# Kernel optimization log

Measured on AMD Instinct MI355X. Metric: run time of the kernel, lower is better.

Reference implementation:

```python
import jax, jax.numpy as jnp
import numpy as np

# ---- config (mirrors DecodeSSDPredictions init kwargs) ----
IMG_H, IMG_W = 512, 512
NMS_MAX = 100          # nms_max_output_size: greedy NMS iterations
CONF_T = 0.5           # confidence_threshold
IOU_T = 0.35           # iou_threshold
NUM_PRED = 10          # num_predictions (final top-k)
B, N_BOXES, N_CLASSES = 32, 24564, 81  # class 0 = background


def setup_inputs() -> dict:
    key = jax.random.key(0)
    k1, k2, k3, k4 = jax.random.split(key, 4)
    # class confidences: softmax of sharp logits so a fraction pass conf>=0.5
    cls = jax.nn.softmax(jax.random.normal(k1, (B, N_BOXES, N_CLASSES), jnp.float32) * 3.0, axis=-1)
    # predicted offsets (cx, cy, log w, log h deltas)
    offsets = jax.random.normal(k2, (B, N_BOXES, 4), jnp.float32) * 0.5
    # anchor priors: centers in (0,1), sizes in (0.05, 0.3)
    cxcy = jax.random.uniform(k3, (B, N_BOXES, 2), jnp.float32, 0.05, 0.95)
    wh = jax.random.uniform(k4, (B, N_BOXES, 2), jnp.float32, 0.05, 0.30)
    variances = jnp.broadcast_to(jnp.array([0.1, 0.1, 0.2, 0.2], jnp.float32), (B, N_BOXES, 4))
    y_pred = jnp.concatenate([cls, offsets, cxcy, wh, variances], axis=-1)  # [B, N, C+12]
    return {"y_pred": y_pred}


def _iou(boxes, box):
    # boxes: [N,4] corners (xmin,ymin,xmax,ymax); box: [4]
    iw = jnp.clip(jnp.minimum(boxes[:, 2], box[2]) - jnp.maximum(boxes[:, 0], box[0]), 0.0)
    ih = jnp.clip(jnp.minimum(boxes[:, 3], box[3]) - jnp.maximum(boxes[:, 1], box[1]), 0.0)
    inter = iw * ih
    area_b = (boxes[:, 2] - boxes[:, 0]) * (boxes[:, 3] - boxes[:, 1])
    area_q = (box[2] - box[0]) * (box[3] - box[1])
    return inter / (area_b + area_q - inter + 1e-12)


def _per_item(rows6):
    # rows6: [N, 6] = (class_id, score, xmin, ymin, xmax, ymax)
    neg_inf = jnp.float32(-jnp.inf)
    valid = (rows6[:, 0] != 0) & (rows6[:, 1] >= CONF_T)  # drop background + low conf
    scores0 = jnp.where(valid, rows6[:, 1], neg_inf)
    boxes = rows6[:, 2:6]

    def body(i, carry):
        alive, kept_idx, kept_sc = carry
        idx = jnp.argmax(alive)
        best = alive[idx]
        ok = best > neg_inf
        kept_idx = kept_idx.at[i].set(jnp.where(ok, idx.astype(jnp.int32), -1))
        kept_sc = kept_sc.at[i].set(jnp.where(ok, best, neg_inf))
        # suppress overlapping boxes (incl. the selected one, iou=1 > thr)
        sup = _iou(boxes, boxes[idx]) > IOU_T
        alive = jnp.where(ok & sup, neg_inf, alive)
        return alive, kept_idx, kept_sc

    carry0 = (scores0,
              jnp.full((NMS_MAX,), -1, jnp.int32),
              jnp.full((NMS_MAX,), neg_inf, jnp.float32))
    _, kept_idx, kept_sc = jax.lax.fori_loop(0, NMS_MAX, body, carry0)

    kept_rows = rows6[jnp.clip(kept_idx, 0)]            # [NMS_MAX, 6]
    top_sc, top_i = jax.lax.top_k(kept_sc, NUM_PRED)    # final top-k by score
    out = kept_rows[top_i]
    return jnp.where(jnp.isfinite(top_sc)[:, None], out, 0.0)


def reference(y_pred):
    cls = y_pred[..., :-12]
    # SSD box decode
    cx = y_pred[..., -12] * y_pred[..., -4] * y_pred[..., -6] + y_pred[..., -8]
    cy = y_pred[..., -11] * y_pred[..., -3] * y_pred[..., -5] + y_pred[..., -7]
    w = jnp.exp(y_pred[..., -10] * y_pred[..., -2]) * y_pred[..., -6]
    h = jnp.exp(y_pred[..., -9] * y_pred[..., -1]) * y_pred[..., -5]
    xmin = (cx - 0.5 * w) * IMG_W
    ymin = (cy - 0.5 * h) * IMG_H
    xmax = (cx + 0.5 * w) * IMG_W
    ymax = (cy + 0.5 * h) * IMG_H
    class_id = jnp.argmax(cls, axis=-1).astype(y_pred.dtype)
    score = jnp.max(cls, axis=-1)
    rows = jnp.stack([class_id, score, xmin, ymin, xmax, ymax], axis=-1)  # [B, N, 6]
    return jax.vmap(_per_item)(rows)  # [B, NUM_PRED, 6]
```

## Files before the change

kernel.cpp:

```cpp
#include <hip/hip_runtime.h>
#include <math.h>

#define B 32
#define NBOX 24564
#define NCLS 81
#define ROWLEN 93
#define CONF_T 0.5f
#define IOU_T 0.35f
#define NUM_PRED 10
#define IMG_W 512.0f
#define IMG_H 512.0f

#define BPB 64
#define K1_THREADS 256
#define NBLK ((NBOX + BPB - 1) / BPB)

#define K2_THREADS 1024
#define NPER ((NBOX + K2_THREADS - 1) / K2_THREADS)

__global__ __launch_bounds__(K1_THREADS) void decode_kernel(
    const float* __restrict__ y, float4* __restrict__ boxes,
    float* __restrict__ scores, float* __restrict__ clsid)
{
    __shared__ float lds[BPB * ROWLEN];
    int bid  = blockIdx.x;
    int b    = bid / NBLK;
    int blk  = bid % NBLK;
    int box0 = blk * BPB;
    int nb   = NBOX - box0; if (nb > BPB) nb = BPB;
    int elems = nb * ROWLEN;
    const float* src = y + ((size_t)b * NBOX + box0) * ROWLEN;
    for (int k = threadIdx.x; k < elems; k += K1_THREADS)
        lds[k] = src[k];
    __syncthreads();

    int q  = threadIdx.x & 3;
    int bl = threadIdx.x >> 2;
    if (bl >= nb) return;
    const float* row = &lds[bl * ROWLEN];

    float best = -INFINITY; int bci = 0x7fffffff;
    for (int c = q; c < NCLS; c += 4) {
        float v = row[c];
        if (v > best) { best = v; bci = c; }
    }
    #pragma unroll
    for (int m = 1; m <= 2; m <<= 1) {
        float ov = __shfl_xor(best, m, 64);
        int   oi = __shfl_xor(bci,  m, 64);
        if (ov > best || (ov == best && oi < bci)) { best = ov; bci = oi; }
    }

    if (q == 0) {
        const float* t = row + NCLS;
        float off0=t[0], off1=t[1], off2=t[2], off3=t[3];
        float acx =t[4], acy =t[5], aw  =t[6], ah  =t[7];
        float v0  =t[8], v1  =t[9], v2  =t[10], v3 =t[11];
        float cx = off0 * v0 * aw + acx;
        float cy = off1 * v1 * ah + acy;
        float w  = expf(off2 * v2) * aw;
        float h  = expf(off3 * v3) * ah;
        float4 bx;
        bx.x = (cx - 0.5f * w) * IMG_W;
        bx.y = (cy - 0.5f * h) * IMG_H;
        bx.z = (cx + 0.5f * w) * IMG_W;
        bx.w = (cy + 0.5f * h) * IMG_H;
        size_t g = (size_t)b * NBOX + box0 + bl;
        boxes[g] = bx;
        clsid[g] = (float)bci;
        bool valid = (bci != 0) && (best >= CONF_T);
        scores[g] = valid ? best : -INFINITY;
    }
}

__global__ __launch_bounds__(K2_THREADS) void nms_kernel(
    const float4* __restrict__ boxes, const float* __restrict__ scores,
    const float* __restrict__ clsid, float* __restrict__ out)
{
    __shared__ float rv[K2_THREADS];
    __shared__ int   ri[K2_THREADS];
    __shared__ float sb[4];
    int b   = blockIdx.x;
    int tid = threadIdx.x;
    const float*  sc_g = scores + (size_t)b * NBOX;
    const float4* bx_g = boxes  + (size_t)b * NBOX;

    float sc[NPER];
    #pragma unroll
    for (int j = 0; j < NPER; j++) {
        int g = j * K2_THREADS + tid;
        sc[j] = (g < NBOX) ? sc_g[g] : -INFINITY;
    }

    for (int r = 0; r < NUM_PRED; r++) {
        float v = -INFINITY; int idx = 0x7fffffff;
        #pragma unroll
        for (int j = 0; j < NPER; j++) {
            int g = j * K2_THREADS + tid;
            if (sc[j] > v || (sc[j] == v && g < idx)) { v = sc[j]; idx = g; }
        }
        rv[tid] = v; ri[tid] = idx;
        __syncthreads();
        for (int s = K2_THREADS / 2; s > 0; s >>= 1) {
            if (tid < s) {
                float ov = rv[tid + s]; int oi = ri[tid + s];
                if (ov > rv[tid] || (ov == rv[tid] && oi < ri[tid])) {
                    rv[tid] = ov; ri[tid] = oi;
                }
            }
            __syncthreads();
        }
        float bv = rv[0]; int bi = ri[0];
        bool ok = (bv > -INFINITY);

        if (tid == 0) {
            float* o = out + ((size_t)b * NUM_PRED + r) * 6;
            if (ok) {
                float4 bb = bx_g[bi];
                sb[0] = bb.x; sb[1] = bb.y; sb[2] = bb.z; sb[3] = bb.w;
                o[0] = clsid[(size_t)b * NBOX + bi];
                o[1] = bv;
                o[2] = bb.x; o[3] = bb.y; o[4] = bb.z; o[5] = bb.w;
            } else {
                for (int k = 0; k < 6; k++) o[k] = 0.0f;
            }
        }
        __syncthreads();

        if (ok) {
            float qx0 = sb[0], qy0 = sb[1], qx1 = sb[2], qy1 = sb[3];
            float aq = (qx1 - qx0) * (qy1 - qy0);
            #pragma unroll
            for (int j = 0; j < NPER; j++) {
                int g = j * K2_THREADS + tid;
                if (g < NBOX && sc[j] > -INFINITY) {
                    float4 p = bx_g[g];
                    float iw = fmaxf(fminf(p.z, qx1) - fmaxf(p.x, qx0), 0.0f);
                    float ih = fmaxf(fminf(p.w, qy1) - fmaxf(p.y, qy0), 0.0f);
                    float inter = iw * ih;
                    float ab = (p.z - p.x) * (p.w - p.y);
                    float iou = inter / (ab + aq - inter + 1e-12f);
                    if (iou > IOU_T) sc[j] = -INFINITY;
                }
            }
        }
        __syncthreads();
    }
}

extern "C" void kernel_launch(void* const* d_in, const int* in_sizes, int n_in,
                              void* d_out, int out_size, void* d_ws, size_t ws_size,
                              hipStream_t stream) {
    const float* y = (const float*)d_in[0];
    float* out = (float*)d_out;
    float* ws  = (float*)d_ws;
    float4* boxes  = (float4*)ws;
    float*  scores = ws + (size_t)B * NBOX * 4;
    float*  clsidp = scores + (size_t)B * NBOX;

    decode_kernel<<<B * NBLK, K1_THREADS, 0, stream>>>(y, boxes, scores, clsidp);
    nms_kernel<<<B, K2_THREADS, 0, stream>>>(boxes, scores, clsidp, out);
}
```

Measured before the change: 503.5 us.

## Compact valid candidates with atomics and use wave-shuffle argmax in NMS

The decode kernel now appends only boxes that pass the class and confidence filter to a per-image compacted list. Each wavefront takes one atomicAdd on a counter and uses ballot/popcount to place its boxes, and the row loads go to LDS as float4. The NMS kernel scans only the compacted candidates, and it replaces the 1024-wide shared-memory tree reduction with wave shuffles plus a small second-level reduction. It also exits early once no candidates remain. The aim is to cut global reads and barrier-heavy reductions in the serial NMS loop, but candidate order now depends on atomic order, so index-based tie-breaking between equal scores is lost.

Measured after the change: 904.1 us. 1.8x slower.

```diff
diff --git a/kernel.cpp b/kernel.cpp
--- a/kernel.cpp
+++ b/kernel.cpp
@@ -15,34 +15,38 @@
 #define K1_THREADS 256
 #define NBLK ((NBOX + BPB - 1) / BPB)
 
-#define K2_THREADS 1024
-#define NPER ((NBOX + K2_THREADS - 1) / K2_THREADS)
+#define K2T 1024
+#define NPER ((NBOX + K2T - 1) / K2T)
 
 __global__ __launch_bounds__(K1_THREADS) void decode_kernel(
-    const float* __restrict__ y, float4* __restrict__ boxes,
-    float* __restrict__ scores, float* __restrict__ clsid)
+    const float* __restrict__ y, float4* __restrict__ candBox,
+    float2* __restrict__ candSc, int* __restrict__ cnt)
 {
-    __shared__ float lds[BPB * ROWLEN];
+    __shared__ float4 lds4[(BPB * ROWLEN) / 4];
+    float* lds = (float*)lds4;
     int bid  = blockIdx.x;
     int b    = bid / NBLK;
     int blk  = bid % NBLK;
     int box0 = blk * BPB;
     int nb   = NBOX - box0; if (nb > BPB) nb = BPB;
-    int elems = nb * ROWLEN;
-    const float* src = y + ((size_t)b * NBOX + box0) * ROWLEN;
-    for (int k = threadIdx.x; k < elems; k += K1_THREADS)
-        lds[k] = src[k];
+    int n4   = (nb * ROWLEN) / 4;
+    const float4* src = (const float4*)(y + ((size_t)b * NBOX + box0) * ROWLEN);
+    for (int k = threadIdx.x; k < n4; k += K1_THREADS)
+        lds4[k] = src[k];
     __syncthreads();
 
     int q  = threadIdx.x & 3;
     int bl = threadIdx.x >> 2;
-    if (bl >= nb) return;
+    int lane = threadIdx.x & 63;
+    bool have = (bl < nb);
     const float* row = &lds[bl * ROWLEN];
 
     float best = -INFINITY; int bci = 0x7fffffff;
-    for (int c = q; c < NCLS; c += 4) {
-        float v = row[c];
-        if (v > best) { best = v; bci = c; }
+    if (have) {
+        for (int c = q; c < NCLS; c += 4) {
+            float v = row[c];
+            if (v > best) { best = v; bci = c; }
+        }
     }
     #pragma unroll
     for (int m = 1; m <= 2; m <<= 1) {
@@ -51,97 +55,111 @@
         if (ov > best || (ov == best && oi < bci)) { best = ov; bci = oi; }
     }
 
-    if (q == 0) {
+    float4 bx; bool valid = false;
+    if (have && q == 0) {
         const float* t = row + NCLS;
-        float off0=t[0], off1=t[1], off2=t[2], off3=t[3];
-        float acx =t[4], acy =t[5], aw  =t[6], ah  =t[7];
-        float v0  =t[8], v1  =t[9], v2  =t[10], v3 =t[11];
-        float cx = off0 * v0 * aw + acx;
-        float cy = off1 * v1 * ah + acy;
-        float w  = expf(off2 * v2) * aw;
-        float h  = expf(off3 * v3) * ah;
-        float4 bx;
+        float cx = t[0] * t[8]  * t[6] + t[4];
+        float cy = t[1] * t[9]  * t[7] + t[5];
+        float w  = expf(t[2] * t[10]) * t[6];
+        float h  = expf(t[3] * t[11]) * t[7];
         bx.x = (cx - 0.5f * w) * IMG_W;
         bx.y = (cy - 0.5f * h) * IMG_H;
         bx.z = (cx + 0.5f * w) * IMG_W;
         bx.w = (cy + 0.5f * h) * IMG_H;
-        size_t g = (size_t)b * NBOX + box0 + bl;
-        boxes[g] = bx;
-        clsid[g] = (float)bci;
-        bool valid = (bci != 0) && (best >= CONF_T);
-        scores[g] = valid ? best : -INFINITY;
+        valid = (bci != 0) && (best >= CONF_T);
+    }
+
+    unsigned long long mask = __ballot(valid);
+    int n = __popcll(mask);
+    int base = 0;
+    if (lane == 0 && n) base = atomicAdd(&cnt[b], n);
+    base = __shfl(base, 0, 64);
+    if (valid) {
+        int slot = base + __popcll(mask & ((1ull << lane) - 1ull));
+        size_t g = (size_t)b * NBOX + slot;
+        candBox[g] = bx;
+        candSc[g]  = make_float2(best, (float)bci);
     }
 }
 
-__global__ __launch_bounds__(K2_THREADS) void nms_kernel(
-    const float4* __restrict__ boxes, const float* __restrict__ scores,
-    const float* __restrict__ clsid, float* __restrict__ out)
+__global__ __launch_bounds__(K2T) void nms_kernel(
+    const float4* __restrict__ candBox, const float2* __restrict__ candSc,
+    const int* __restrict__ cnt, float* __restrict__ out)
 {
-    __shared__ float rv[K2_THREADS];
-    __shared__ int   ri[K2_THREADS];
-    __shared__ float sb[4];
-    int b   = blockIdx.x;
-    int tid = threadIdx.x;
-    const float*  sc_g = scores + (size_t)b * NBOX;
-    const float4* bx_g = boxes  + (size_t)b * NBOX;
+    __shared__ float pv[16];
+    __shared__ int   pi[16];
+    __shared__ float bvS;
+    __shared__ int   biS;
+    int b = blockIdx.x, tid = threadIdx.x;
+    int lane = tid & 63, wid = tid >> 6;
+    int M = cnt[b]; if (M > NBOX) M = NBOX;
+    const float4* bxp = candBox + (size_t)b * NBOX;
+    const float2* sgp = candSc  + (size_t)b * NBOX;
 
     float sc[NPER];
     #pragma unroll
     for (int j = 0; j < NPER; j++) {
-        int g = j * K2_THREADS + tid;
-        sc[j] = (g < NBOX) ? sc_g[g] : -INFINITY;
+        int g = j * K2T + tid;
+        sc[j] = (g < M) ? sgp[g].x : -INFINITY;
     }
 
     for (int r = 0; r < NUM_PRED; r++) {
-        float v = -INFINITY; int idx = 0x7fffffff;
+        float v = -INFINITY; int idx = -1;
         #pragma unroll
         for (int j = 0; j < NPER; j++) {
-            int g = j * K2_THREADS + tid;
-            if (sc[j] > v || (sc[j] == v && g < idx)) { v = sc[j]; idx = g; }
+            int g = j * K2T + tid;
+            if (sc[j] > v) { v = sc[j]; idx = g; }
         }
-        rv[tid] = v; ri[tid] = idx;
+        #pragma unroll
+        for (int m = 1; m < 64; m <<= 1) {
+            float ov = __shfl_xor(v, m, 64);
+            int   oi = __shfl_xor(idx, m, 64);
+            if (ov > v) { v = ov; idx = oi; }
+        }
+        if (lane == 0) { pv[wid] = v; pi[wid] = idx; }
         __syncthreads();
-        for (int s = K2_THREADS / 2; s > 0; s >>= 1) {
-            if (tid < s) {
-                float ov = rv[tid + s]; int oi = ri[tid + s];
-                if (ov > rv[tid] || (ov == rv[tid] && oi < ri[tid])) {
-                    rv[tid] = ov; ri[tid] = oi;
+        if (wid == 0) {
+            float v2 = (lane < 16) ? pv[lane] : -INFINITY;
+            int   i2 = (lane < 16) ? pi[lane] : -1;
+            #pragma unroll
+            for (int m = 1; m < 16; m <<= 1) {
+                float ov = __shfl_xor(v2, m, 64);
+                int   oi = __shfl_xor(i2, m, 64);
+                if (ov > v2) { v2 = ov; i2 = oi; }
+            }
+            if (lane == 0) { bvS = v2; biS = i2; }
+        }
+        __syncthreads();
+        float bv = bvS; int bi = biS;
+
+        if (!(bv > -INFINITY)) {
+            if (tid == 0) {
+                for (int rr = r; rr < NUM_PRED; rr++) {
+                    float* o = out + ((size_t)b * NUM_PRED + rr) * 6;
+                    for (int k = 0; k < 6; k++) o[k] = 0.0f;
                 }
             }
-            __syncthreads();
+            break;
         }
-        float bv = rv[0]; int bi = ri[0];
-        bool ok = (bv > -INFINITY);
 
+        float4 qb = bxp[bi];
         if (tid == 0) {
             float* o = out + ((size_t)b * NUM_PRED + r) * 6;
-            if (ok) {
-                float4 bb = bx_g[bi];
-                sb[0] = bb.x; sb[1] = bb.y; sb[2] = bb.z; sb[3] = bb.w;
-                o[0] = clsid[(size_t)b * NBOX + bi];
-                o[1] = bv;
-                o[2] = bb.x; o[3] = bb.y; o[4] = bb.z; o[5] = bb.w;
-            } else {
-                for (int k = 0; k < 6; k++) o[k] = 0.0f;
-            }
+            o[0] = sgp[bi].y; o[1] = bv;
+            o[2] = qb.x; o[3] = qb.y; o[4] = qb.z; o[5] = qb.w;
         }
-        __syncthreads();
-
-        if (ok) {
-            float qx0 = sb[0], qy0 = sb[1], qx1 = sb[2], qy1 = sb[3];
-            float aq = (qx1 - qx0) * (qy1 - qy0);
-            #pragma unroll
-            for (int j = 0; j < NPER; j++) {
-                int g = j * K2_THREADS + tid;
-                if (g < NBOX && sc[j] > -INFINITY) {
-                    float4 p = bx_g[g];
-                    float iw = fmaxf(fminf(p.z, qx1) - fmaxf(p.x, qx0), 0.0f);
-                    float ih = fmaxf(fminf(p.w, qy1) - fmaxf(p.y, qy0), 0.0f);
-                    float inter = iw * ih;
-                    float ab = (p.z - p.x) * (p.w - p.y);
-                    float iou = inter / (ab + aq - inter + 1e-12f);
-                    if (iou > IOU_T) sc[j] = -INFINITY;
-                }
+        float aq = (qb.z - qb.x) * (qb.w - qb.y);
+        #pragma unroll
+        for (int j = 0; j < NPER; j++) {
+            int g = j * K2T + tid;
+            if (g < M && sc[j] > -INFINITY) {
+                float4 p = bxp[g];
+                float iw = fmaxf(fminf(p.z, qb.z) - fmaxf(p.x, qb.x), 0.0f);
+                float ih = fmaxf(fminf(p.w, qb.w) - fmaxf(p.y, qb.y), 0.0f);
+                float inter = iw * ih;
+                float ab = (p.z - p.x) * (p.w - p.y);
+                float iou = inter / (ab + aq - inter + 1e-12f);
+                if (iou > IOU_T) sc[j] = -INFINITY;
             }
         }
         __syncthreads();
@@ -153,11 +171,12 @@
                               hipStream_t stream) {
     const float* y = (const float*)d_in[0];
     float* out = (float*)d_out;
-    float* ws  = (float*)d_ws;
-    float4* boxes  = (float4*)ws;
-    float*  scores = ws + (size_t)B * NBOX * 4;
-    float*  clsidp = scores + (size_t)B * NBOX;
+    char* ws = (char*)d_ws;
+    float4* candBox = (float4*)ws;
+    float2* candSc  = (float2*)(ws + (size_t)B * NBOX * sizeof(float4));
+    int*    cnt     = (int*)(ws + (size_t)B * NBOX * (sizeof(float4) + sizeof(float2)));
 
-    decode_kernel<<<B * NBLK, K1_THREADS, 0, stream>>>(y, boxes, scores, clsidp);
-    nms_kernel<<<B, K2_THREADS, 0, stream>>>(boxes, scores, clsidp, out);
+    hipMemsetAsync(cnt, 0, B * sizeof(int), stream);
+    decode_kernel<<<B * NBLK, K1_THREADS, 0, stream>>>(y, candBox, candSc, cnt);
+    nms_kernel<<<B, K2T, 0, stream>>>(candBox, candSc, cnt, out);
 }
```
